# Kernel tuning notes

Hardware: AMD Instinct MI355X
Metric: run time of the kernel (lower is better)

The kernel has to match this reference:

```python
import jax, jax.numpy as jnp
import numpy as np

MARGIN = 0.1
NEG_INF = -1e30


def _l2norm(x):
    return x / jnp.linalg.norm(x, axis=1, keepdims=True)


def setup_inputs() -> dict:
    key = jax.random.key(0)
    ks = jax.random.split(key, 6)
    d, nNeg, Q = 128, 10, 32
    triplet_len = nNeg + 2
    n = Q * triplet_len            # 384
    m = 65536                      # XBM memory bank size
    V = 2048                       # image-id space
    P, Nn = 10, 25                 # pos / hard-neg list lengths per query
    inputs_col = _l2norm(jax.random.normal(ks[0], (n, d), dtype=jnp.float32))
    inputs_row = _l2norm(jax.random.normal(ks[1], (m, d), dtype=jnp.float32))
    targets_row = jax.random.randint(ks[2], (m,), 0, V, dtype=jnp.int64)
    qidxs = jnp.arange(Q, dtype=jnp.int64) + V  # unique query ids, disjoint from db ids
    targets_col = jax.random.randint(ks[3], (n,), 0, V, dtype=jnp.int64)
    targets_col = targets_col.at[jnp.arange(0, n, triplet_len)].set(qidxs)
    pidxs = jax.random.randint(ks[4], (Q, P), 0, V, dtype=jnp.int64)
    nnegs = jax.random.randint(ks[5], (Q, Nn), 0, V, dtype=jnp.int64)
    return {"inputs_col": inputs_col, "inputs_row": inputs_row,
            "targets_col": targets_col, "targets_row": targets_row,
            "qidxs": qidxs, "pidxs": pidxs, "nnegs": nnegs, "nNeg": nNeg}


def reference(inputs_col, inputs_row, targets_col, targets_row, qidxs, pidxs, nnegs, nNeg):
    n = inputs_col.shape[0]
    triplet_len = nNeg + 2
    query_list = jnp.arange(0, n, triplet_len)          # [Q]
    Q = query_list.shape[0]
    query_idx = targets_col[query_list]                 # [Q]

    sim_mat = inputs_col @ inputs_row.T                 # [n, m]
    sims = sim_mat[query_list]                          # [Q, m]

    # per-query lookup of pos / neg id lists (qidxs are unique)
    qidx_local = jnp.argmax(qidxs[None, :] == query_idx[:, None], axis=1)
    this_pidx = pidxs[qidx_local]                       # [Q, P]
    this_nneg = nnegs[qidx_local]                       # [Q, Nn]

    # from_batch handling (only possible when shapes match; here memory-bank case)
    if targets_col.shape[0] == targets_row.shape[0]:
        fb = jnp.all(targets_col == targets_row)
        trc = jnp.where(fb, targets_row.at[query_list].set(-1), targets_row)
    else:
        fb = None
        trc = targets_row

    # isin masks, vectorized across queries: [Q, m]
    pos_mask = jnp.any(targets_row[None, :, None] == this_pidx[:, None, :], axis=-1)
    neg_mask = ~jnp.any(trc[None, :, None] == this_nneg[:, None, :], axis=-1)
    if fb is not None:
        neg_mask = jnp.where(fb, neg_mask.at[:, query_list].set(False), neg_mask)

    # sort was only used to read the max -> masked max suffices
    pos_max = jnp.max(jnp.where(pos_mask, sims, NEG_INF), axis=1)   # [Q]
    neg_max = jnp.max(jnp.where(neg_mask, sims, NEG_INF), axis=1)   # [Q]

    pos_sel = pos_mask & (sims < neg_max[:, None] + MARGIN)
    neg_sel = neg_mask & (sims > jnp.maximum(0.4, pos_max)[:, None] - MARGIN)

    pos_cnt = jnp.sum(pos_sel, axis=1)
    neg_cnt = jnp.sum(neg_sel, axis=1)
    pos_loss = jnp.where(pos_cnt > 0,
                         jnp.sum(jnp.where(pos_sel, 1.0 - sims, 0.0), axis=1) / jnp.maximum(pos_cnt, 1),
                         0.0)
    neg_loss = jnp.where(neg_cnt > 0,
                         jnp.sum(jnp.where(neg_sel, sims, 0.0), axis=1) / jnp.maximum(neg_cnt, 1),
                         0.0)

    has_pos = jnp.any(pos_mask, axis=1)                 # whole block skipped if no positives
    loss = jnp.sum(jnp.where(has_pos, pos_loss + neg_loss, 0.0)) / Q
    return loss
```

## Files before the change

### kernel.cpp

```cpp
#include <hip/hip_runtime.h>

#define NEG_INF_F (-1e30f)
#define MARGIN_F 0.1f
#define TABN 4096
#define BR 128

__device__ __forceinline__ unsigned fkey(float f) {
    unsigned b = __float_as_uint(f);
    return (b & 0x80000000u) ? ~b : (b | 0x80000000u);
}
__device__ __forceinline__ float fdec(unsigned k) {
    unsigned b = (k & 0x80000000u) ? (k ^ 0x80000000u) : ~k;
    return __uint_as_float(b);
}

__global__ __launch_bounds__(256) void setup_kernel(
    const float* __restrict__ inputs_col,
    const int* __restrict__ targets_col,
    const int* __restrict__ qidxs,
    const int* __restrict__ pidxs,
    const int* __restrict__ nnegs,
    unsigned* __restrict__ ptab,
    unsigned* __restrict__ ntab,
    float* __restrict__ qT,
    unsigned* __restrict__ qkeys,
    float* __restrict__ accums,
    int d, int Q, int P, int Nn, int triplet_len)
{
    __shared__ int qmap[32];
    const int tid = threadIdx.x;

    if (tid < Q) {
        int t = targets_col[tid * triplet_len];
        int l = 0;
        for (int i = Q - 1; i >= 0; --i) if (qidxs[i] == t) l = i;
        qmap[tid] = l;
    }
    for (int i = tid; i < TABN; i += 256) { ptab[i] = 0u; ntab[i] = 0u; }
    if (tid < 2 * Q) qkeys[tid] = fkey(NEG_INF_F);
    if (tid < 8 * Q) accums[tid] = 0.f;
    __syncthreads();

    for (int i = tid; i < Q * P; i += 256) {
        int q = i / P, k = i - q * P;
        int id = pidxs[qmap[q] * P + k];
        if ((unsigned)id < TABN) atomicOr(&ptab[id], 1u << q);
    }
    for (int i = tid; i < Q * Nn; i += 256) {
        int q = i / Nn, k = i - q * Nn;
        int id = nnegs[qmap[q] * Nn + k];
        if ((unsigned)id < TABN) atomicOr(&ntab[id], 1u << q);
    }
    for (int i = tid; i < d * Q; i += 256) {
        int dd = i >> 5, q = i & 31;
        qT[i] = inputs_col[(size_t)(q * triplet_len) * d + dd];
    }
}

__global__ __launch_bounds__(256) void sims_kernel(
    const float* __restrict__ qT,
    const float* __restrict__ rows,
    const int* __restrict__ targets_row,
    const unsigned* __restrict__ ptab,
    const unsigned* __restrict__ ntab,
    float* __restrict__ sims,
    unsigned* __restrict__ posbits,
    unsigned* __restrict__ negbits,
    unsigned* __restrict__ qkeys,
    int m, int d)
{
    __shared__ float qv[128][32];
    __shared__ float rt[32][132];
    __shared__ unsigned pbm[BR], nbm[BR];
    __shared__ unsigned spk[32], snk[32];
    const int tid = threadIdx.x;
    const int j0 = blockIdx.x * BR;

    for (int i = tid; i < 128 * 32; i += 256) qv[i >> 5][i & 31] = qT[i];
    if (tid < 32) { spk[tid] = fkey(NEG_INF_F); snk[tid] = fkey(NEG_INF_F); }
    if (tid < BR) {
        int j = j0 + tid;
        unsigned pb = 0u, nb = 0u;
        if (j < m) {
            int t = targets_row[j];
            if ((unsigned)t < TABN) { pb = ptab[t]; nb = ~ntab[t]; }
            else                    { nb = ~0u; }
        }
        pbm[tid] = pb; nbm[tid] = nb;
        if (j < m) { posbits[j] = pb; negbits[j] = nb; }
    }

    const int qg = tid & 7;
    const int rg = tid >> 3;
    const int jj = tid >> 3;
    const int kk = tid & 7;

    float acc[4][4];
#pragma unroll
    for (int a = 0; a < 4; ++a)
#pragma unroll
        for (int b = 0; b < 4; ++b) acc[a][b] = 0.f;

    for (int kc = 0; kc < 128; kc += 32) {
        __syncthreads();
#pragma unroll
        for (int p = 0; p < 4; ++p) {
            int j = j0 + jj + 32 * p;
            int jc = (j < m) ? j : (m - 1);
            float4 v = *(const float4*)&rows[(size_t)jc * 128 + kc + 4 * kk];
            rt[4 * kk + 0][jj + 32 * p] = v.x;
            rt[4 * kk + 1][jj + 32 * p] = v.y;
            rt[4 * kk + 2][jj + 32 * p] = v.z;
            rt[4 * kk + 3][jj + 32 * p] = v.w;
        }
        __syncthreads();
#pragma unroll
        for (int k = 0; k < 32; ++k) {
            float4 qf = *(const float4*)&qv[kc + k][qg * 4];
            float4 rf = *(const float4*)&rt[k][rg * 4];
            const float* qp = (const float*)&qf;
            const float* rp = (const float*)&rf;
#pragma unroll
            for (int qi = 0; qi < 4; ++qi)
#pragma unroll
                for (int ri = 0; ri < 4; ++ri)
                    acc[qi][ri] = fmaf(qp[qi], rp[ri], acc[qi][ri]);
        }
    }

    unsigned pb[4], nb[4];
#pragma unroll
    for (int r = 0; r < 4; ++r) { pb[r] = pbm[rg * 4 + r]; nb[r] = nbm[rg * 4 + r]; }

    const bool full = (j0 + BR <= m);
#pragma unroll
    for (int qi = 0; qi < 4; ++qi) {
        const int q = qg * 4 + qi;
        float pmax = NEG_INF_F, nmax = NEG_INF_F;
#pragma unroll
        for (int r = 0; r < 4; ++r) {
            if ((pb[r] >> q) & 1u) pmax = fmaxf(pmax, acc[qi][r]);
            if ((nb[r] >> q) & 1u) nmax = fmaxf(nmax, acc[qi][r]);
        }
#pragma unroll
        for (int off = 32; off >= 8; off >>= 1) {
            pmax = fmaxf(pmax, __shfl_down(pmax, off));
            nmax = fmaxf(nmax, __shfl_down(nmax, off));
        }
        if ((tid & 63) < 8) {
            atomicMax(&spk[q], fkey(pmax));
            atomicMax(&snk[q], fkey(nmax));
        }
        if (full) {
            *(float4*)&sims[(size_t)q * m + j0 + rg * 4] =
                make_float4(acc[qi][0], acc[qi][1], acc[qi][2], acc[qi][3]);
        } else {
#pragma unroll
            for (int r = 0; r < 4; ++r) {
                int j = j0 + rg * 4 + r;
                if (j < m) sims[(size_t)q * m + j] = acc[qi][r];
            }
        }
    }
    __syncthreads();
    if (tid < 32) {
        atomicMax(&qkeys[tid * 2],     spk[tid]);
        atomicMax(&qkeys[tid * 2 + 1], snk[tid]);
    }
}

__global__ __launch_bounds__(256) void select_kernel(
    const float* __restrict__ sims,
    const unsigned* __restrict__ posbits,
    const unsigned* __restrict__ negbits,
    const unsigned* __restrict__ qkeys,
    float* __restrict__ accums,
    int m)
{
    const int q = blockIdx.y;
    const float pos_max = fdec(qkeys[q * 2]);
    const float neg_max = fdec(qkeys[q * 2 + 1]);
    const float posThr = neg_max + MARGIN_F;
    const float negThr = fmaxf(0.4f, pos_max) - MARGIN_F;

    const int chunk = (m + gridDim.x - 1) / gridDim.x;
    const int jb = blockIdx.x * chunk;
    const int je = min(m, jb + chunk);

    float ps = 0.f, pc = 0.f, ns = 0.f, nc = 0.f, pmc = 0.f;
    for (int j = jb + threadIdx.x; j < je; j += blockDim.x) {
        float s = sims[(size_t)q * m + j];
        unsigned pm = (posbits[j] >> q) & 1u;
        unsigned nm = (negbits[j] >> q) & 1u;
        pmc += (float)pm;
        if (pm && s < posThr) { ps += 1.f - s; pc += 1.f; }
        if (nm && s > negThr) { ns += s;       nc += 1.f; }
    }
#pragma unroll
    for (int off = 32; off; off >>= 1) {
        ps  += __shfl_down(ps, off);
        pc  += __shfl_down(pc, off);
        ns  += __shfl_down(ns, off);
        nc  += __shfl_down(nc, off);
        pmc += __shfl_down(pmc, off);
    }
    if ((threadIdx.x & 63) == 0) {
        atomicAdd(&accums[q * 8 + 0], ps);
        atomicAdd(&accums[q * 8 + 1], pc);
        atomicAdd(&accums[q * 8 + 2], ns);
        atomicAdd(&accums[q * 8 + 3], nc);
        atomicAdd(&accums[q * 8 + 4], pmc);
    }
}

__global__ void finalize_kernel(const float* __restrict__ accums,
                                float* __restrict__ out, int Q)
{
    int q = threadIdx.x;
    float v = 0.f;
    if (q < Q) {
        float ps  = accums[q * 8 + 0];
        float pc  = accums[q * 8 + 1];
        float ns  = accums[q * 8 + 2];
        float nc  = accums[q * 8 + 3];
        float pmc = accums[q * 8 + 4];
        float pl = (pc > 0.f) ? ps / pc : 0.f;
        float nl = (nc > 0.f) ? ns / nc : 0.f;
        v = (pmc > 0.f) ? (pl + nl) : 0.f;
    }
#pragma unroll
    for (int off = 32; off; off >>= 1) v += __shfl_down(v, off);
    if (q == 0) out[0] = v / (float)Q;
}

extern "C" void kernel_launch(void* const* d_in, const int* in_sizes, int n_in,
                              void* d_out, int out_size, void* d_ws, size_t ws_size,
                              hipStream_t stream)
{
    const float* inputs_col = (const float*)d_in[0];
    const float* inputs_row = (const float*)d_in[1];
    const int* targets_col  = (const int*)d_in[2];
    const int* targets_row  = (const int*)d_in[3];
    const int* qidxs        = (const int*)d_in[4];
    const int* pidxs        = (const int*)d_in[5];
    const int* nnegs        = (const int*)d_in[6];

    const int n  = in_sizes[2];
    const int m  = in_sizes[3];
    const int Q  = in_sizes[4];
    const int P  = in_sizes[5] / Q;
    const int Nn = in_sizes[6] / Q;
    const int d  = in_sizes[0] / n;
    const int triplet_len = n / Q;

    char* ws = (char*)d_ws;
    float* sims = (float*)ws;
    size_t off = (size_t)Q * m * sizeof(float);
    unsigned* posbits = (unsigned*)(ws + off); off += (size_t)m * 4;
    unsigned* negbits = (unsigned*)(ws + off); off += (size_t)m * 4;
    unsigned* ptab    = (unsigned*)(ws + off); off += (size_t)TABN * 4;
    unsigned* ntab    = (unsigned*)(ws + off); off += (size_t)TABN * 4;
    float* qT         = (float*)(ws + off);    off += (size_t)d * Q * 4;
    unsigned* qkeys   = (unsigned*)(ws + off); off += (size_t)Q * 2 * 4;
    float* accums     = (float*)(ws + off);    off += (size_t)Q * 8 * 4;

    setup_kernel<<<1, 256, 0, stream>>>(inputs_col, targets_col, qidxs, pidxs, nnegs,
                                        ptab, ntab, qT, qkeys, accums,
                                        d, Q, P, Nn, triplet_len);

    const int nb = (m + BR - 1) / BR;
    sims_kernel<<<nb, 256, 0, stream>>>(qT, inputs_row, targets_row, ptab, ntab,
                                        sims, posbits, negbits, qkeys, m, d);

    dim3 gsel(32, Q);
    select_kernel<<<gsel, 256, 0, stream>>>(sims, posbits, negbits, qkeys, accums, m);

    finalize_kernel<<<1, 64, 0, stream>>>((const float*)accums, (float*)d_out, Q);
}
```

Before: 162.7 us.

## Fuse sims, selection and finalize into one persistent kernel with grid barrier

Merges the similarity, selection and finalize kernels into a single kernel. Similarity values stay in registers instead of being written as a Q×m matrix and read back, and a software grid-wide barrier publishes the per-query max thresholds between the two phases. Tile size doubles to 256 rows with 512 threads, giving 256 blocks that must all be co-resident for the spin barrier to be safe. A last-block counter then computes the final loss. This removes the large sims round trip through global memory and two kernel launches, but risks deadlock if not all blocks are resident, and it hardcodes Q=32.

```diff
diff --git a/kernel.cpp b/kernel.cpp
--- a/kernel.cpp
+++ b/kernel.cpp
@@ -3,7 +3,8 @@
 #define NEG_INF_F (-1e30f)
 #define MARGIN_F 0.1f
 #define TABN 4096
-#define BR 128
+#define BR 256
+#define NT 512
 
 __device__ __forceinline__ unsigned fkey(float f) {
     unsigned b = __float_as_uint(f);
@@ -23,8 +24,8 @@
     unsigned* __restrict__ ptab,
     unsigned* __restrict__ ntab,
     float* __restrict__ qT,
-    unsigned* __restrict__ qkeys,
     float* __restrict__ accums,
+    unsigned* __restrict__ bar,
     int d, int Q, int P, int Nn, int triplet_len)
 {
     __shared__ int qmap[32];
@@ -37,8 +38,8 @@
         qmap[tid] = l;
     }
     for (int i = tid; i < TABN; i += 256) { ptab[i] = 0u; ntab[i] = 0u; }
-    if (tid < 2 * Q) qkeys[tid] = fkey(NEG_INF_F);
-    if (tid < 8 * Q) accums[tid] = 0.f;
+    if (tid < 160) accums[tid] = 0.f;
+    if (tid < 2) bar[tid] = 0u;
     __syncthreads();
 
     for (int i = tid; i < Q * P; i += 256) {
@@ -57,43 +58,59 @@
     }
 }
 
-__global__ __launch_bounds__(256) void sims_kernel(
+__device__ __forceinline__ void gsync(unsigned* cnt, unsigned nblk) {
+    __syncthreads();
+    if (threadIdx.x == 0) {
+        __threadfence();
+        atomicAdd(cnt, 1u);
+        while (__hip_atomic_load(cnt, __ATOMIC_RELAXED, __HIP_MEMORY_SCOPE_AGENT) < nblk)
+            __builtin_amdgcn_s_sleep(2);
+        __threadfence();
+    }
+    __syncthreads();
+}
+
+__global__ __launch_bounds__(NT, 2) void fused_kernel(
     const float* __restrict__ qT,
     const float* __restrict__ rows,
     const int* __restrict__ targets_row,
     const unsigned* __restrict__ ptab,
     const unsigned* __restrict__ ntab,
-    float* __restrict__ sims,
-    unsigned* __restrict__ posbits,
-    unsigned* __restrict__ negbits,
-    unsigned* __restrict__ qkeys,
-    int m, int d)
+    float* __restrict__ gmax,
+    float* __restrict__ accums,
+    unsigned* __restrict__ bar,
+    float* __restrict__ out,
+    int m, int nb)
 {
     __shared__ float qv[128][32];
-    __shared__ float rt[32][132];
+    __shared__ float rt[32][261];
     __shared__ unsigned pbm[BR], nbm[BR];
     __shared__ unsigned spk[32], snk[32];
+    __shared__ float thr[2][32];
+    __shared__ float wpart[8][32][5];
+    __shared__ int islast;
+
     const int tid = threadIdx.x;
-    const int j0 = blockIdx.x * BR;
-
-    for (int i = tid; i < 128 * 32; i += 256) qv[i >> 5][i & 31] = qT[i];
+    const int bid = blockIdx.x;
+    const int j0 = bid * BR;
+
+    for (int i = tid; i < 128 * 32; i += NT) qv[i >> 5][i & 31] = qT[i];
     if (tid < 32) { spk[tid] = fkey(NEG_INF_F); snk[tid] = fkey(NEG_INF_F); }
     if (tid < BR) {
         int j = j0 + tid;
-        unsigned pb = 0u, nb = 0u;
+        unsigned pb = 0u, nbv = 0u;
         if (j < m) {
             int t = targets_row[j];
-            if ((unsigned)t < TABN) { pb = ptab[t]; nb = ~ntab[t]; }
-            else                    { nb = ~0u; }
-        }
-        pbm[tid] = pb; nbm[tid] = nb;
-        if (j < m) { posbits[j] = pb; negbits[j] = nb; }
+            if ((unsigned)t < TABN) { pb = ptab[t]; nbv = ~ntab[t]; }
+            else                    { nbv = ~0u; }
+        }
+        pbm[tid] = pb; nbm[tid] = nbv;
     }
 
     const int qg = tid & 7;
     const int rg = tid >> 3;
+    const int kk = tid & 7;
     const int jj = tid >> 3;
-    const int kk = tid & 7;
 
     float acc[4][4];
 #pragma unroll
@@ -105,13 +122,13 @@
         __syncthreads();
 #pragma unroll
         for (int p = 0; p < 4; ++p) {
-            int j = j0 + jj + 32 * p;
+            int j = j0 + jj + 64 * p;
             int jc = (j < m) ? j : (m - 1);
             float4 v = *(const float4*)&rows[(size_t)jc * 128 + kc + 4 * kk];
-            rt[4 * kk + 0][jj + 32 * p] = v.x;
-            rt[4 * kk + 1][jj + 32 * p] = v.y;
-            rt[4 * kk + 2][jj + 32 * p] = v.z;
-            rt[4 * kk + 3][jj + 32 * p] = v.w;
+            rt[4 * kk + 0][jj + 64 * p] = v.x;
+            rt[4 * kk + 1][jj + 64 * p] = v.y;
+            rt[4 * kk + 2][jj + 64 * p] = v.z;
+            rt[4 * kk + 3][jj + 64 * p] = v.w;
         }
         __syncthreads();
 #pragma unroll
@@ -128,19 +145,18 @@
         }
     }
 
-    unsigned pb[4], nb[4];
-#pragma unroll
-    for (int r = 0; r < 4; ++r) { pb[r] = pbm[rg * 4 + r]; nb[r] = nbm[rg * 4 + r]; }
-
-    const bool full = (j0 + BR <= m);
+    unsigned pb[4], nbr[4];
+#pragma unroll
+    for (int r = 0; r < 4; ++r) { pb[r] = pbm[rg * 4 + r]; nbr[r] = nbm[rg * 4 + r]; }
+
 #pragma unroll
     for (int qi = 0; qi < 4; ++qi) {
         const int q = qg * 4 + qi;
         float pmax = NEG_INF_F, nmax = NEG_INF_F;
 #pragma unroll
         for (int r = 0; r < 4; ++r) {
-            if ((pb[r] >> q) & 1u) pmax = fmaxf(pmax, acc[qi][r]);
-            if ((nb[r] >> q) & 1u) nmax = fmaxf(nmax, acc[qi][r]);
+            if ((pb[r] >> q) & 1u)  pmax = fmaxf(pmax, acc[qi][r]);
+            if ((nbr[r] >> q) & 1u) nmax = fmaxf(nmax, acc[qi][r]);
         }
 #pragma unroll
         for (int off = 32; off >= 8; off >>= 1) {
@@ -151,86 +167,92 @@
             atomicMax(&spk[q], fkey(pmax));
             atomicMax(&snk[q], fkey(nmax));
         }
-        if (full) {
-            *(float4*)&sims[(size_t)q * m + j0 + rg * 4] =
-                make_float4(acc[qi][0], acc[qi][1], acc[qi][2], acc[qi][3]);
-        } else {
-#pragma unroll
-            for (int r = 0; r < 4; ++r) {
-                int j = j0 + rg * 4 + r;
-                if (j < m) sims[(size_t)q * m + j] = acc[qi][r];
+    }
+    __syncthreads();
+    if (tid < 64) {
+        int side = tid >> 5, q = tid & 31;
+        gmax[(size_t)tid * nb + bid] = fdec(side ? snk[q] : spk[q]);
+    }
+
+    gsync(&bar[0], (unsigned)nb);
+
+    {
+        int p = tid >> 3, c = tid & 7;
+        float mv = NEG_INF_F;
+        for (int b = c; b < nb; b += 8) mv = fmaxf(mv, gmax[(size_t)p * nb + b]);
+#pragma unroll
+        for (int msk = 1; msk <= 4; msk <<= 1) mv = fmaxf(mv, __shfl_xor(mv, msk));
+        if (c == 0) thr[p >> 5][p & 31] = mv;
+    }
+    __syncthreads();
+
+    const int wave = tid >> 6, lane = tid & 63;
+#pragma unroll
+    for (int qi = 0; qi < 4; ++qi) {
+        const int q = qg * 4 + qi;
+        const float posThr = thr[1][q] + MARGIN_F;
+        const float negThr = fmaxf(0.4f, thr[0][q]) - MARGIN_F;
+        float ps = 0.f, pc = 0.f, ns = 0.f, nc = 0.f, pmc = 0.f;
+#pragma unroll
+        for (int r = 0; r < 4; ++r) {
+            float s = acc[qi][r];
+            unsigned pm = (pb[r] >> q) & 1u;
+            unsigned nm = (nbr[r] >> q) & 1u;
+            pmc += (float)pm;
+            if (pm && s < posThr) { ps += 1.f - s; pc += 1.f; }
+            if (nm && s > negThr) { ns += s;       nc += 1.f; }
+        }
+#pragma unroll
+        for (int off = 32; off >= 8; off >>= 1) {
+            ps  += __shfl_down(ps, off);
+            pc  += __shfl_down(pc, off);
+            ns  += __shfl_down(ns, off);
+            nc  += __shfl_down(nc, off);
+            pmc += __shfl_down(pmc, off);
+        }
+        if (lane < 8) {
+            wpart[wave][lane * 4 + qi][0] = ps;
+            wpart[wave][lane * 4 + qi][1] = pc;
+            wpart[wave][lane * 4 + qi][2] = ns;
+            wpart[wave][lane * 4 + qi][3] = nc;
+            wpart[wave][lane * 4 + qi][4] = pmc;
+        }
+    }
+    __syncthreads();
+    if (tid < 160) {
+        float v = 0.f;
+#pragma unroll
+        for (int w = 0; w < 8; ++w) v += wpart[w][tid / 5][tid % 5];
+        atomicAdd(&accums[tid], v);
+    }
+
+    __syncthreads();
+    if (tid == 0) {
+        __threadfence();
+        unsigned old = atomicAdd(&bar[1], 1u);
+        islast = (old == (unsigned)(nb - 1)) ? 1 : 0;
+    }
+    __syncthreads();
+    if (islast) {
+        if (tid == 0) __threadfence();
+        __syncthreads();
+        if (tid < 64) {
+            float v = 0.f;
+            if (tid < 32) {
+                float psv = accums[tid * 5 + 0];
+                float pcv = accums[tid * 5 + 1];
+                float nsv = accums[tid * 5 + 2];
+                float ncv = accums[tid * 5 + 3];
+                float pmc = accums[tid * 5 + 4];
+                float pl = (pcv > 0.f) ? psv / pcv : 0.f;
+                float nl = (ncv > 0.f) ? nsv / ncv : 0.f;
+                v = (pmc > 0.f) ? (pl + nl) : 0.f;
             }
-        }
-    }
-    __syncthreads();
-    if (tid < 32) {
-        atomicMax(&qkeys[tid * 2],     spk[tid]);
-        atomicMax(&qkeys[tid * 2 + 1], snk[tid]);
-    }
-}
-
-__global__ __launch_bounds__(256) void select_kernel(
-    const float* __restrict__ sims,
-    const unsigned* __restrict__ posbits,
-    const unsigned* __restrict__ negbits,
-    const unsigned* __restrict__ qkeys,
-    float* __restrict__ accums,
-    int m)
-{
-    const int q = blockIdx.y;
-    const float pos_max = fdec(qkeys[q * 2]);
-    const float neg_max = fdec(qkeys[q * 2 + 1]);
-    const float posThr = neg_max + MARGIN_F;
-    const float negThr = fmaxf(0.4f, pos_max) - MARGIN_F;
-
-    const int chunk = (m + gridDim.x - 1) / gridDim.x;
-    const int jb = blockIdx.x * chunk;
-    const int je = min(m, jb + chunk);
-
-    float ps = 0.f, pc = 0.f, ns = 0.f, nc = 0.f, pmc = 0.f;
-    for (int j = jb + threadIdx.x; j < je; j += blockDim.x) {
-        float s = sims[(size_t)q * m + j];
-        unsigned pm = (posbits[j] >> q) & 1u;
-        unsigned nm = (negbits[j] >> q) & 1u;
-        pmc += (float)pm;
-        if (pm && s < posThr) { ps += 1.f - s; pc += 1.f; }
-        if (nm && s > negThr) { ns += s;       nc += 1.f; }
-    }
-#pragma unroll
-    for (int off = 32; off; off >>= 1) {
-        ps  += __shfl_down(ps, off);
-        pc  += __shfl_down(pc, off);
-        ns  += __shfl_down(ns, off);
-        nc  += __shfl_down(nc, off);
-        pmc += __shfl_down(pmc, off);
-    }
-    if ((threadIdx.x & 63) == 0) {
-        atomicAdd(&accums[q * 8 + 0], ps);
-        atomicAdd(&accums[q * 8 + 1], pc);
-        atomicAdd(&accums[q * 8 + 2], ns);
-        atomicAdd(&accums[q * 8 + 3], nc);
-        atomicAdd(&accums[q * 8 + 4], pmc);
-    }
-}
-
-__global__ void finalize_kernel(const float* __restrict__ accums,
-                                float* __restrict__ out, int Q)
-{
-    int q = threadIdx.x;
-    float v = 0.f;
-    if (q < Q) {
-        float ps  = accums[q * 8 + 0];
-        float pc  = accums[q * 8 + 1];
-        float ns  = accums[q * 8 + 2];
-        float nc  = accums[q * 8 + 3];
-        float pmc = accums[q * 8 + 4];
-        float pl = (pc > 0.f) ? ps / pc : 0.f;
-        float nl = (nc > 0.f) ? ns / nc : 0.f;
-        v = (pmc > 0.f) ? (pl + nl) : 0.f;
-    }
-#pragma unroll
-    for (int off = 32; off; off >>= 1) v += __shfl_down(v, off);
-    if (q == 0) out[0] = v / (float)Q;
+#pragma unroll
+            for (int off = 32; off; off >>= 1) v += __shfl_down(v, off);
+            if (tid == 0) out[0] = v / 32.0f;
+        }
+    }
 }
 
 extern "C" void kernel_launch(void* const* d_in, const int* in_sizes, int n_in,
@@ -246,34 +268,29 @@
     const int* nnegs        = (const int*)d_in[6];
 
     const int n  = in_sizes[2];
-    const int m  = in_sizes[3];
+    int m        = in_sizes[3];
     const int Q  = in_sizes[4];
     const int P  = in_sizes[5] / Q;
     const int Nn = in_sizes[6] / Q;
     const int d  = in_sizes[0] / n;
     const int triplet_len = n / Q;
 
+    int nb = (m + BR - 1) / BR;
+
     char* ws = (char*)d_ws;
-    float* sims = (float*)ws;
-    size_t off = (size_t)Q * m * sizeof(float);
-    unsigned* posbits = (unsigned*)(ws + off); off += (size_t)m * 4;
-    unsigned* negbits = (unsigned*)(ws + off); off += (size_t)m * 4;
-    unsigned* ptab    = (unsigned*)(ws + off); off += (size_t)TABN * 4;
-    unsigned* ntab    = (unsigned*)(ws + off); off += (size_t)TABN * 4;
-    float* qT         = (float*)(ws + off);    off += (size_t)d * Q * 4;
-    unsigned* qkeys   = (unsigned*)(ws + off); off += (size_t)Q * 2 * 4;
-    float* accums     = (float*)(ws + off);    off += (size_t)Q * 8 * 4;
+    size_t off = 0;
+    unsigned* ptab = (unsigned*)(ws + off); off += (size_t)TABN * 4;
+    unsigned* ntab = (unsigned*)(ws + off); off += (size_t)TABN * 4;
+    float* qT      = (float*)(ws + off);    off += (size_t)d * Q * 4;
+    float* gmax    = (float*)(ws + off);    off += (size_t)64 * nb * 4;
+    float* accums  = (float*)(ws + off);    off += (size_t)160 * 4;
+    unsigned* bar  = (unsigned*)(ws + off); off += 2 * 4;
+    float* out     = (float*)d_out;
 
     setup_kernel<<<1, 256, 0, stream>>>(inputs_col, targets_col, qidxs, pidxs, nnegs,
-                                        ptab, ntab, qT, qkeys, accums,
+                                        ptab, ntab, qT, accums, bar,
                                         d, Q, P, Nn, triplet_len);
 
-    const int nb = (m + BR - 1) / BR;
-    sims_kernel<<<nb, 256, 0, stream>>>(qT, inputs_row, targets_row, ptab, ntab,
-                                        sims, posbits, negbits, qkeys, m, d);
-
-    dim3 gsel(32, Q);
-    select_kernel<<<gsel, 256, 0, stream>>>(sims, posbits, negbits, qkeys, accums, m);
-
-    finalize_kernel<<<1, 64, 0, stream>>>((const float*)accums, (float*)d_out, Q);
-}
+    fused_kernel<<<nb, NT, 0, stream>>>(qT, inputs_row, targets_row, ptab, ntab,
+                                        gmax, accums, bar, out, m, nb);
+}
```

After: 138.3 us. 15.0% less time.
